# Kernel optimization log

Measured on AMD Instinct MI355X. Metric: run time of the kernel, lower is better.

## Reference

```python
import jax, jax.numpy as jnp
import numpy as np

DIM = 1024
HEADS = 16
DIM_HEAD = 64


def setup_inputs() -> dict:
    key = jax.random.key(0)
    ks = jax.random.split(key, 6)
    b, n = 2, 2048
    x = jax.random.normal(ks[0], (b, n, DIM), dtype=jnp.float32)
    gamma = jnp.ones((DIM,), dtype=jnp.float32)
    w_qkv = jax.random.normal(ks[1], (DIM, 3 * HEADS * DIM_HEAD), dtype=jnp.float32) * (DIM ** -0.5)
    w_gates = jax.random.normal(ks[2], (DIM, HEADS), dtype=jnp.float32) * (DIM ** -0.5)
    b_gates = jnp.zeros((HEADS,), dtype=jnp.float32)
    w_out = jax.random.normal(ks[3], (HEADS * DIM_HEAD, DIM), dtype=jnp.float32) * ((HEADS * DIM_HEAD) ** -0.5)
    freqs = jax.random.uniform(ks[4], (DIM_HEAD // 2,), dtype=jnp.float32)
    return {"x": x, "gamma": gamma, "w_qkv": w_qkv, "w_gates": w_gates,
            "b_gates": b_gates, "w_out": w_out, "freqs": freqs}


def _rotate_half(t):
    # interleaved pairs: (x1, x2) -> (-x2, x1)
    tp = t.reshape(t.shape[:-1] + (t.shape[-1] // 2, 2))
    x1, x2 = tp[..., 0], tp[..., 1]
    return jnp.stack((-x2, x1), axis=-1).reshape(t.shape)


def reference(x, gamma, w_qkv, w_gates, b_gates, w_out, freqs):
    b, n, d = x.shape
    # RMSNorm variant: divide by L2 norm, scale by gamma * sqrt(dim)
    xn = x / jnp.linalg.norm(x, axis=-1, keepdims=True)
    xn = xn * gamma * (d ** 0.5)
    # QKV projection: (b, n, 3*H*D) -> q,k,v each (b, h, n, dh)
    qkv = xn @ w_qkv
    qkv = qkv.reshape(b, n, 3, HEADS, DIM_HEAD).transpose(2, 0, 3, 1, 4)
    q, k, v = qkv[0], qkv[1], qkv[2]
    # Inline RoPE (interleaved): freqs (n, dh)
    pos = jnp.arange(n, dtype=freqs.dtype)
    f = jnp.repeat(pos[:, None] * freqs[None, :], 2, axis=-1)  # (n, dh)
    cos_f, sin_f = jnp.cos(f), jnp.sin(f)
    q = q * cos_f + _rotate_half(q) * sin_f
    k = k * cos_f + _rotate_half(k) * sin_f
    # SDPA
    scale = DIM_HEAD ** -0.5
    scores = jnp.einsum('bhqd,bhkd->bhqk', q, k) * scale
    attn = jax.nn.softmax(scores, axis=-1)
    out = jnp.einsum('bhqk,bhkd->bhqd', attn, v)  # (b, h, n, dh)
    # per-head sigmoid gate from normalized input
    gates = xn @ w_gates + b_gates  # (b, n, h)
    out = out * jax.nn.sigmoid(gates.transpose(0, 2, 1))[..., None]
    # merge heads and output projection
    out = out.transpose(0, 2, 1, 3).reshape(b, n, HEADS * DIM_HEAD)
    return out @ w_out
```

## Files before the change

### kernel.cpp

```cpp
#include <hip/hip_runtime.h>

typedef __bf16 bf16_t;
typedef __bf16 bf16x8 __attribute__((ext_vector_type(8)));
typedef __bf16 bf16x4 __attribute__((ext_vector_type(4)));
typedef float f32x4 __attribute__((ext_vector_type(4)));

#define B_  2
#define N_  2048
#define D_  1024
#define H_  16
#define DH_ 64

#define GLL16(g, l) __builtin_amdgcn_global_load_lds( \
    (const __attribute__((address_space(1))) void*)(g), \
    (__attribute__((address_space(3))) void*)(l), 16, 0, 0)

__global__ __launch_bounds__(256) void k_rmsnorm(const float* __restrict__ x,
    const float* __restrict__ gamma, bf16_t* __restrict__ xn) {
  int row = blockIdx.x;
  const float4* xr = (const float4*)(x + (size_t)row * D_);
  int tid = threadIdx.x;
  float4 v = xr[tid];
  float ss = v.x*v.x + v.y*v.y + v.z*v.z + v.w*v.w;
  #pragma unroll
  for (int off = 32; off > 0; off >>= 1) ss += __shfl_down(ss, off);
  __shared__ float red[4];
  if ((tid & 63) == 0) red[tid >> 6] = ss;
  __syncthreads();
  float scale = 32.0f * rsqrtf(red[0] + red[1] + red[2] + red[3]);
  float4 g = ((const float4*)gamma)[tid];
  bf16x4 o;
  o[0] = (bf16_t)(v.x * scale * g.x);
  o[1] = (bf16_t)(v.y * scale * g.y);
  o[2] = (bf16_t)(v.z * scale * g.z);
  o[3] = (bf16_t)(v.w * scale * g.w);
  *(bf16x4*)(xn + (size_t)row * D_ + tid * 4) = o;
}

__global__ __launch_bounds__(256) void k_transpose_cvt(const float* __restrict__ W,
    bf16_t* __restrict__ Wt, int R, int C) {
  __shared__ float tile[32][33];
  int c0 = blockIdx.x * 32, r0 = blockIdx.y * 32;
  int tx = threadIdx.x & 31, ty = threadIdx.x >> 5;
  #pragma unroll
  for (int i = 0; i < 4; ++i) {
    int r = ty + i * 8;
    tile[r][tx] = W[(size_t)(r0 + r) * C + c0 + tx];
  }
  __syncthreads();
  #pragma unroll
  for (int i = 0; i < 4; ++i) {
    int rr = ty + i * 8;
    Wt[(size_t)(c0 + rr) * R + r0 + tx] = (bf16_t)tile[tx][rr];
  }
}

template<bool OUT_BF16>
__global__ __launch_bounds__(256) void k_gemm_bt(const bf16_t* __restrict__ A,
    const bf16_t* __restrict__ Bt, void* __restrict__ Cp, int M, int N, int K) {
  constexpr int BK = 32;
  __shared__ __align__(16) bf16_t As[128 * BK];
  __shared__ __align__(16) bf16_t Bs[128 * BK];
  int tid = threadIdx.x, wave = tid >> 6, lane = tid & 63;
  int l16 = lane & 15, quad = lane >> 4;
  int bm = blockIdx.x * 128, bn = blockIdx.y * 128;
  int wm = (wave >> 1) * 64, wn = (wave & 1) * 64;
  int srow = wave * 32 + (lane >> 2);
  int scol = (lane & 3) * 8;
  const bf16_t* gA0 = &A [(size_t)(bm + srow)      * K + scol];
  const bf16_t* gA1 = &A [(size_t)(bm + srow + 16) * K + scol];
  const bf16_t* gB0 = &Bt[(size_t)(bn + srow)      * K + scol];
  const bf16_t* gB1 = &Bt[(size_t)(bn + srow + 16) * K + scol];
  bf16_t* lA0 = &As[(wave * 32)      * BK];
  bf16_t* lA1 = &As[(wave * 32 + 16) * BK];
  bf16_t* lB0 = &Bs[(wave * 32)      * BK];
  bf16_t* lB1 = &Bs[(wave * 32 + 16) * BK];
  f32x4 acc[4][4] = {};
  for (int k0 = 0; k0 < K; k0 += BK) {
    GLL16(gA0 + k0, lA0);
    GLL16(gA1 + k0, lA1);
    GLL16(gB0 + k0, lB0);
    GLL16(gB1 + k0, lB1);
    __syncthreads();
    bf16x8 af[4], bfr[4];
    #pragma unroll
    for (int t = 0; t < 4; ++t) {
      af[t]  = *(const bf16x8*)&As[(wm + t * 16 + l16) * BK + quad * 8];
      bfr[t] = *(const bf16x8*)&Bs[(wn + t * 16 + l16) * BK + quad * 8];
    }
    #pragma unroll
    for (int mt = 0; mt < 4; ++mt)
      #pragma unroll
      for (int nt = 0; nt < 4; ++nt)
        acc[mt][nt] = __builtin_amdgcn_mfma_f32_16x16x32_bf16(af[mt], bfr[nt], acc[mt][nt], 0, 0, 0);
    __syncthreads();
  }
  #pragma unroll
  for (int mt = 0; mt < 4; ++mt)
    #pragma unroll
    for (int nt = 0; nt < 4; ++nt)
      #pragma unroll
      for (int r = 0; r < 4; ++r) {
        int row = bm + wm + mt * 16 + quad * 4 + r;
        int col = bn + wn + nt * 16 + l16;
        float v = acc[mt][nt][r];
        if (OUT_BF16) ((bf16_t*)Cp)[(size_t)row * N + col] = (bf16_t)v;
        else          ((float*)Cp)[(size_t)row * N + col] = v;
      }
}

__global__ __launch_bounds__(256) void k_rope(const bf16_t* __restrict__ qkvb,
    const float* __restrict__ freqs, bf16_t* __restrict__ Qb, bf16_t* __restrict__ Kb) {
  int row = blockIdx.x, b = row >> 11, n = row & 2047;
  __shared__ float cs[32], sn[32];
  int tid = threadIdx.x;
  if (tid < 32) { float f = (float)n * freqs[tid]; cs[tid] = cosf(f); sn[tid] = sinf(f); }
  __syncthreads();
  const bf16_t* src = qkvb + (size_t)row * 3072;
  #pragma unroll
  for (int it = 0; it < 2; ++it) {
    int p = tid + 256 * it;
    int h = p >> 5, j = p & 31;
    size_t dst = ((size_t)(b * H_ + h) * N_ + n) * DH_ + 2 * j;
    float c = cs[j], s = sn[j];
    {
      float v0 = (float)src[h * 64 + 2 * j], v1 = (float)src[h * 64 + 2 * j + 1];
      union { bf16_t q[2]; unsigned u; } pk;
      pk.q[0] = (bf16_t)((v0 * c - v1 * s) * 0.125f);
      pk.q[1] = (bf16_t)((v1 * c + v0 * s) * 0.125f);
      *(unsigned*)&Qb[dst] = pk.u;
    }
    {
      float v0 = (float)src[1024 + h * 64 + 2 * j], v1 = (float)src[1024 + h * 64 + 2 * j + 1];
      union { bf16_t q[2]; unsigned u; } pk;
      pk.q[0] = (bf16_t)(v0 * c - v1 * s);
      pk.q[1] = (bf16_t)(v1 * c + v0 * s);
      *(unsigned*)&Kb[dst] = pk.u;
    }
  }
}

__global__ __launch_bounds__(256) void k_vtrans(const bf16_t* __restrict__ qkvb,
    bf16_t* __restrict__ Vb) {
  __shared__ bf16_t Vs[64][72];
  int bh = blockIdx.x, nt = blockIdx.y;
  int b = bh >> 4, h = bh & 15;
  int n0 = nt * 64;
  int tid = threadIdx.x;
  #pragma unroll
  for (int it = 0; it < 2; ++it) {
    int chunk = tid + 256 * it;
    int nl = chunk >> 3, c = (chunk & 7) * 8;
    *(bf16x8*)&Vs[nl][c] =
        *(const bf16x8*)&qkvb[(size_t)(b * N_ + n0 + nl) * 3072 + 2048 + h * 64 + c];
  }
  __syncthreads();
  #pragma unroll
  for (int it = 0; it < 2; ++it) {
    int chunk = tid + 256 * it;
    int d = chunk >> 3, nc = (chunk & 7) * 8;
    bf16x8 o;
    #pragma unroll
    for (int jj = 0; jj < 8; ++jj) o[jj] = Vs[nc + jj][d];
    *(bf16x8*)&Vb[((size_t)bh * DH_ + d) * N_ + n0 + nc] = o;
  }
}

__global__ __launch_bounds__(256) void k_gates(const bf16_t* __restrict__ xn,
    const float* __restrict__ wg, const float* __restrict__ bg,
    float* __restrict__ gsig) {
  int row = blockIdx.x;
  int tid = threadIdx.x;
  int h = tid & 15, seg = tid >> 4;
  const bf16_t* xr = xn + (size_t)row * D_;
  float part = 0.f;
  #pragma unroll 8
  for (int j = 0; j < 64; ++j) {
    int i = seg * 64 + j;
    part += (float)xr[i] * wg[i * 16 + h];
  }
  __shared__ float red[16][17];
  red[seg][h] = part;
  __syncthreads();
  if (tid < 16) {
    float s = bg[tid];
    #pragma unroll
    for (int sg = 0; sg < 16; ++sg) s += red[sg][tid];
    gsig[(size_t)row * 16 + tid] = 1.0f / (1.0f + __expf(-s));
  }
}

__global__ __launch_bounds__(256) void k_flash(const bf16_t* __restrict__ Qb,
    const bf16_t* __restrict__ Kb, const bf16_t* __restrict__ Vb,
    const float* __restrict__ gsig, bf16_t* __restrict__ Ao) {
  __shared__ __align__(16) bf16_t Ks[64 * 72];
  __shared__ __align__(16) bf16_t Vt[64 * 72];
  __shared__ __align__(16) bf16_t Ps[4][32 * 72];
  int bh = blockIdx.y, b = bh >> 4, h = bh & 15;
  int tid = threadIdx.x, wave = tid >> 6, lane = tid & 63;
  int l16 = lane & 15, quad = lane >> 4;
  int qw = blockIdx.x * 128 + wave * 32;
  const bf16_t* Qh = Qb + (size_t)bh * N_ * DH_;
  const bf16_t* Kh = Kb + (size_t)bh * N_ * DH_;
  const bf16_t* Vh = Vb + (size_t)bh * DH_ * N_;
  bf16_t* Pw = Ps[wave];
  bf16x8 qf[2][2];
  #pragma unroll
  for (int qt = 0; qt < 2; ++qt)
    #pragma unroll
    for (int hf = 0; hf < 2; ++hf)
      qf[qt][hf] = *(const bf16x8*)&Qh[(size_t)(qw + qt * 16 + l16) * DH_ + hf * 32 + quad * 8];
  f32x4 accO[2][4] = {};
  float lsum[2] = {0.f, 0.f};
  int sk = tid >> 3;
  int sc = (tid & 7) * 8;
  for (int k0 = 0; k0 < N_; k0 += 64) {
    *(bf16x8*)&Ks[sk * 72 + sc]        = *(const bf16x8*)&Kh[(size_t)(k0 + sk) * DH_ + sc];
    *(bf16x8*)&Ks[(sk + 32) * 72 + sc] = *(const bf16x8*)&Kh[(size_t)(k0 + sk + 32) * DH_ + sc];
    *(bf16x8*)&Vt[sk * 72 + sc]        = *(const bf16x8*)&Vh[(size_t)sk * N_ + k0 + sc];
    *(bf16x8*)&Vt[(sk + 32) * 72 + sc] = *(const bf16x8*)&Vh[(size_t)(sk + 32) * N_ + k0 + sc];
    __syncthreads();
    f32x4 st[4][2];
    #pragma unroll
    for (int kt = 0; kt < 4; ++kt) {
      bf16x8 kf0 = *(const bf16x8*)&Ks[(kt * 16 + l16) * 72 + quad * 8];
      bf16x8 kf1 = *(const bf16x8*)&Ks[(kt * 16 + l16) * 72 + 32 + quad * 8];
      #pragma unroll
      for (int qt = 0; qt < 2; ++qt) {
        f32x4 z = {};
        z = __builtin_amdgcn_mfma_f32_16x16x32_bf16(kf0, qf[qt][0], z, 0, 0, 0);
        z = __builtin_amdgcn_mfma_f32_16x16x32_bf16(kf1, qf[qt][1], z, 0, 0, 0);
        st[kt][qt] = z;
      }
    }
    #pragma unroll
    for (int qt = 0; qt < 2; ++qt)
      #pragma unroll
      for (int kt = 0; kt < 4; ++kt) {
        bf16x4 pk;
        #pragma unroll
        for (int r = 0; r < 4; ++r) {
          float p = __expf(st[kt][qt][r] - 8.0f);
          lsum[qt] += p;
          pk[r] = (bf16_t)p;
        }
        *(bf16x4*)&Pw[(qt * 16 + l16) * 72 + kt * 16 + quad * 4] = pk;
      }
    bf16x8 pf[2][2];
    #pragma unroll
    for (int qt = 0; qt < 2; ++qt)
      #pragma unroll
      for (int hf = 0; hf < 2; ++hf)
        pf[qt][hf] = *(const bf16x8*)&Pw[(qt * 16 + l16) * 72 + hf * 32 + quad * 8];
    #pragma unroll
    for (int dt = 0; dt < 4; ++dt)
      #pragma unroll
      for (int hf = 0; hf < 2; ++hf) {
        bf16x8 vf = *(const bf16x8*)&Vt[(dt * 16 + l16) * 72 + hf * 32 + quad * 8];
        #pragma unroll
        for (int qt = 0; qt < 2; ++qt)
          accO[qt][dt] = __builtin_amdgcn_mfma_f32_16x16x32_bf16(pf[qt][hf], vf, accO[qt][dt], 0, 0, 0);
      }
    __syncthreads();
  }
  float lfull[2];
  #pragma unroll
  for (int qt = 0; qt < 2; ++qt) {
    float s = lsum[qt];
    s += __shfl_xor(s, 16);
    s += __shfl_xor(s, 32);
    lfull[qt] = s;
  }
  #pragma unroll
  for (int qt = 0; qt < 2; ++qt)
    #pragma unroll
    for (int r = 0; r < 4; ++r) {
      int qs = quad * 4 + r;
      float l_e = __shfl(lfull[qt], qs);
      int q = qw + qt * 16 + qs;
      float g = gsig[((size_t)b * N_ + q) * H_ + h];
      float ginv = g / l_e;
      #pragma unroll
      for (int dt = 0; dt < 4; ++dt)
        Ao[((size_t)b * N_ + q) * (H_ * DH_) + h * DH_ + dt * 16 + l16] =
            (bf16_t)(accO[qt][dt][r] * ginv);
    }
}

extern "C" void kernel_launch(void* const* d_in, const int* in_sizes, int n_in,
                              void* d_out, int out_size, void* d_ws, size_t ws_size,
                              hipStream_t stream) {
  (void)in_sizes; (void)n_in; (void)out_size; (void)ws_size;
  const float* x      = (const float*)d_in[0];
  const float* gamma  = (const float*)d_in[1];
  const float* w_qkv  = (const float*)d_in[2];
  const float* w_gate = (const float*)d_in[3];
  const float* b_gate = (const float*)d_in[4];
  const float* w_out  = (const float*)d_in[5];
  const float* freqs  = (const float*)d_in[6];
  float* out = (float*)d_out;
  char* ws = (char*)d_ws;
  bf16_t* xn    = (bf16_t*)(ws);
  bf16_t* wqkvT = (bf16_t*)(ws + ((size_t)8  << 20));
  bf16_t* woutT = (bf16_t*)(ws + ((size_t)14 << 20));
  bf16_t* Qb    = (bf16_t*)(ws + ((size_t)16 << 20));
  bf16_t* Kb    = (bf16_t*)(ws + ((size_t)24 << 20));
  bf16_t* Vb    = (bf16_t*)(ws + ((size_t)32 << 20));
  float*  gsig  = (float*) (ws + ((size_t)40 << 20));
  bf16_t* attn  = (bf16_t*)(ws + ((size_t)41 << 20));
  bf16_t* qkvb  = (bf16_t*)(ws + ((size_t)49 << 20));

  k_transpose_cvt<<<dim3(3072 / 32, 1024 / 32), 256, 0, stream>>>(w_qkv, wqkvT, 1024, 3072);
  k_transpose_cvt<<<dim3(1024 / 32, 1024 / 32), 256, 0, stream>>>(w_out, woutT, 1024, 1024);
  k_rmsnorm<<<4096, 256, 0, stream>>>(x, gamma, xn);
  k_gemm_bt<true><<<dim3(32, 24), 256, 0, stream>>>(xn, wqkvT, (void*)qkvb, 4096, 3072, 1024);
  k_rope<<<4096, 256, 0, stream>>>(qkvb, freqs, Qb, Kb);
  k_vtrans<<<dim3(32, 32), 256, 0, stream>>>(qkvb, Vb);
  k_gates<<<4096, 256, 0, stream>>>(xn, w_gate, b_gate, gsig);
  k_flash<<<dim3(16, 32), 256, 0, stream>>>(Qb, Kb, Vb, gsig, attn);
  k_gemm_bt<false><<<dim3(32, 8), 256, 0, stream>>>(attn, woutT, (void*)out, 4096, 1024, 1024);
}
```

Measured before the change: 253.0 us.

## Fuse RoPE and V transpose into QKV GEMM, split flash over keys, retile output GEMM

The QKV GEMM epilogue now applies RoPE to Q and K, using a precomputed cos/sin table, and writes V directly in transposed layout. This removes the bf16 qkv intermediate and the separate rope and vtrans kernels. Flash attention is split into two key halves per query block, which doubles the grid. It writes fp32 partial outputs and row sums, and a new merge kernel combines them and applies the sigmoid gate. The output projection uses 64-row tiles to launch more blocks. The merge adds fp32 partial traffic and is correct only if both halves share the same softmax max reference.

```diff
diff --git a/kernel.cpp b/kernel.cpp
--- a/kernel.cpp
+++ b/kernel.cpp
@@ -14,6 +14,14 @@
 #define GLL16(g, l) __builtin_amdgcn_global_load_lds( \
     (const __attribute__((address_space(1))) void*)(g), \
     (__attribute__((address_space(3))) void*)(l), 16, 0, 0)
+
+__global__ __launch_bounds__(256) void k_trig(const float* __restrict__ freqs,
+    float2* __restrict__ trig) {
+  int i = blockIdx.x * 256 + threadIdx.x;
+  int n = i >> 5, j = i & 31;
+  float f = (float)n * freqs[j];
+  trig[i] = make_float2(cosf(f), sinf(f));
+}
 
 __global__ __launch_bounds__(256) void k_rmsnorm(const float* __restrict__ x,
     const float* __restrict__ gamma, bf16_t* __restrict__ xn) {
@@ -55,10 +63,10 @@
   }
 }
 
-template<bool OUT_BF16>
-__global__ __launch_bounds__(256) void k_gemm_bt(const bf16_t* __restrict__ A,
-    const bf16_t* __restrict__ Bt, void* __restrict__ Cp, int M, int N, int K) {
-  constexpr int BK = 32;
+__global__ __launch_bounds__(256) void k_gemm_qkv(const bf16_t* __restrict__ A,
+    const bf16_t* __restrict__ Bt, const float2* __restrict__ trig,
+    bf16_t* __restrict__ Qb, bf16_t* __restrict__ Kb, bf16_t* __restrict__ Vb) {
+  constexpr int BK = 32, K = 1024;
   __shared__ __align__(16) bf16_t As[128 * BK];
   __shared__ __align__(16) bf16_t Bs[128 * BK];
   int tid = threadIdx.x, wave = tid >> 6, lane = tid & 63;
@@ -95,75 +103,94 @@
         acc[mt][nt] = __builtin_amdgcn_mfma_f32_16x16x32_bf16(af[mt], bfr[nt], acc[mt][nt], 0, 0, 0);
     __syncthreads();
   }
-  #pragma unroll
-  for (int mt = 0; mt < 4; ++mt)
+  int type = bn >> 10;
+  int h = (((bn & 1023) + wn) >> 6);
+  if (type < 2) {
+    bf16_t* dst = (type == 0) ? Qb : Kb;
+    float qsc = (type == 0) ? 0.125f : 1.0f;
+    #pragma unroll
+    for (int nt = 0; nt < 4; ++nt) {
+      int d = nt * 16 + l16;
+      int j = d >> 1;
+      bool odd = (d & 1);
+      #pragma unroll
+      for (int mt = 0; mt < 4; ++mt)
+        #pragma unroll
+        for (int r = 0; r < 4; ++r) {
+          int row = bm + wm + mt * 16 + quad * 4 + r;
+          int b = row >> 11, n = row & 2047;
+          float v = acc[mt][nt][r];
+          float vp = __shfl_xor(v, 1);
+          float2 cs = trig[n * 32 + j];
+          float o = odd ? (v * cs.x + vp * cs.y) : (v * cs.x - vp * cs.y);
+          dst[((size_t)(b * H_ + h) * N_ + n) * DH_ + d] = (bf16_t)(o * qsc);
+        }
+    }
+  } else {
+    #pragma unroll
+    for (int mt = 0; mt < 4; ++mt) {
+      int row0 = bm + wm + mt * 16 + quad * 4;
+      int b = row0 >> 11, n0 = row0 & 2047;
+      #pragma unroll
+      for (int nt = 0; nt < 4; ++nt) {
+        int d = nt * 16 + l16;
+        bf16x4 pk;
+        #pragma unroll
+        for (int r = 0; r < 4; ++r) pk[r] = (bf16_t)acc[mt][nt][r];
+        *(bf16x4*)&Vb[((size_t)(b * H_ + h) * DH_ + d) * N_ + n0] = pk;
+      }
+    }
+  }
+}
+
+__global__ __launch_bounds__(256) void k_gemm_out(const bf16_t* __restrict__ A,
+    const bf16_t* __restrict__ Bt, float* __restrict__ C, int M, int N, int K) {
+  constexpr int BK = 32;
+  __shared__ __align__(16) bf16_t As[64 * BK];
+  __shared__ __align__(16) bf16_t Bs[128 * BK];
+  int tid = threadIdx.x, wave = tid >> 6, lane = tid & 63;
+  int l16 = lane & 15, quad = lane >> 4;
+  int bm = blockIdx.x * 64, bn = blockIdx.y * 128;
+  int wm = (wave >> 1) * 32, wn = (wave & 1) * 64;
+  int srowA = wave * 16 + (lane >> 2);
+  int srowB = wave * 32 + (lane >> 2);
+  int scol = (lane & 3) * 8;
+  const bf16_t* gA0 = &A [(size_t)(bm + srowA)      * K + scol];
+  const bf16_t* gB0 = &Bt[(size_t)(bn + srowB)      * K + scol];
+  const bf16_t* gB1 = &Bt[(size_t)(bn + srowB + 16) * K + scol];
+  bf16_t* lA0 = &As[(wave * 16)      * BK];
+  bf16_t* lB0 = &Bs[(wave * 32)      * BK];
+  bf16_t* lB1 = &Bs[(wave * 32 + 16) * BK];
+  f32x4 acc[2][4] = {};
+  for (int k0 = 0; k0 < K; k0 += BK) {
+    GLL16(gA0 + k0, lA0);
+    GLL16(gB0 + k0, lB0);
+    GLL16(gB1 + k0, lB1);
+    __syncthreads();
+    bf16x8 af[2], bfr[4];
+    #pragma unroll
+    for (int t = 0; t < 2; ++t)
+      af[t] = *(const bf16x8*)&As[(wm + t * 16 + l16) * BK + quad * 8];
+    #pragma unroll
+    for (int t = 0; t < 4; ++t)
+      bfr[t] = *(const bf16x8*)&Bs[(wn + t * 16 + l16) * BK + quad * 8];
+    #pragma unroll
+    for (int mt = 0; mt < 2; ++mt)
+      #pragma unroll
+      for (int nt = 0; nt < 4; ++nt)
+        acc[mt][nt] = __builtin_amdgcn_mfma_f32_16x16x32_bf16(af[mt], bfr[nt], acc[mt][nt], 0, 0, 0);
+    __syncthreads();
+  }
+  #pragma unroll
+  for (int mt = 0; mt < 2; ++mt)
     #pragma unroll
     for (int nt = 0; nt < 4; ++nt)
       #pragma unroll
       for (int r = 0; r < 4; ++r) {
         int row = bm + wm + mt * 16 + quad * 4 + r;
         int col = bn + wn + nt * 16 + l16;
-        float v = acc[mt][nt][r];
-        if (OUT_BF16) ((bf16_t*)Cp)[(size_t)row * N + col] = (bf16_t)v;
-        else          ((float*)Cp)[(size_t)row * N + col] = v;
-      }
-}
-
-__global__ __launch_bounds__(256) void k_rope(const bf16_t* __restrict__ qkvb,
-    const float* __restrict__ freqs, bf16_t* __restrict__ Qb, bf16_t* __restrict__ Kb) {
-  int row = blockIdx.x, b = row >> 11, n = row & 2047;
-  __shared__ float cs[32], sn[32];
-  int tid = threadIdx.x;
-  if (tid < 32) { float f = (float)n * freqs[tid]; cs[tid] = cosf(f); sn[tid] = sinf(f); }
-  __syncthreads();
-  const bf16_t* src = qkvb + (size_t)row * 3072;
-  #pragma unroll
-  for (int it = 0; it < 2; ++it) {
-    int p = tid + 256 * it;
-    int h = p >> 5, j = p & 31;
-    size_t dst = ((size_t)(b * H_ + h) * N_ + n) * DH_ + 2 * j;
-    float c = cs[j], s = sn[j];
-    {
-      float v0 = (float)src[h * 64 + 2 * j], v1 = (float)src[h * 64 + 2 * j + 1];
-      union { bf16_t q[2]; unsigned u; } pk;
-      pk.q[0] = (bf16_t)((v0 * c - v1 * s) * 0.125f);
-      pk.q[1] = (bf16_t)((v1 * c + v0 * s) * 0.125f);
-      *(unsigned*)&Qb[dst] = pk.u;
-    }
-    {
-      float v0 = (float)src[1024 + h * 64 + 2 * j], v1 = (float)src[1024 + h * 64 + 2 * j + 1];
-      union { bf16_t q[2]; unsigned u; } pk;
-      pk.q[0] = (bf16_t)(v0 * c - v1 * s);
-      pk.q[1] = (bf16_t)(v1 * c + v0 * s);
-      *(unsigned*)&Kb[dst] = pk.u;
-    }
-  }
-}
-
-__global__ __launch_bounds__(256) void k_vtrans(const bf16_t* __restrict__ qkvb,
-    bf16_t* __restrict__ Vb) {
-  __shared__ bf16_t Vs[64][72];
-  int bh = blockIdx.x, nt = blockIdx.y;
-  int b = bh >> 4, h = bh & 15;
-  int n0 = nt * 64;
-  int tid = threadIdx.x;
-  #pragma unroll
-  for (int it = 0; it < 2; ++it) {
-    int chunk = tid + 256 * it;
-    int nl = chunk >> 3, c = (chunk & 7) * 8;
-    *(bf16x8*)&Vs[nl][c] =
-        *(const bf16x8*)&qkvb[(size_t)(b * N_ + n0 + nl) * 3072 + 2048 + h * 64 + c];
-  }
-  __syncthreads();
-  #pragma unroll
-  for (int it = 0; it < 2; ++it) {
-    int chunk = tid + 256 * it;
-    int d = chunk >> 3, nc = (chunk & 7) * 8;
-    bf16x8 o;
-    #pragma unroll
-    for (int jj = 0; jj < 8; ++jj) o[jj] = Vs[nc + jj][d];
-    *(bf16x8*)&Vb[((size_t)bh * DH_ + d) * N_ + n0 + nc] = o;
-  }
+        C[(size_t)row * N + col] = acc[mt][nt][r];
+      }
 }
 
 __global__ __launch_bounds__(256) void k_gates(const bf16_t* __restrict__ xn,
@@ -192,11 +219,12 @@
 
 __global__ __launch_bounds__(256) void k_flash(const bf16_t* __restrict__ Qb,
     const bf16_t* __restrict__ Kb, const bf16_t* __restrict__ Vb,
-    const float* __restrict__ gsig, bf16_t* __restrict__ Ao) {
+    float* __restrict__ Op0, float* __restrict__ Op1, float* __restrict__ Lpart) {
   __shared__ __align__(16) bf16_t Ks[64 * 72];
   __shared__ __align__(16) bf16_t Vt[64 * 72];
   __shared__ __align__(16) bf16_t Ps[4][32 * 72];
   int bh = blockIdx.y, b = bh >> 4, h = bh & 15;
+  int split = blockIdx.z;
   int tid = threadIdx.x, wave = tid >> 6, lane = tid & 63;
   int l16 = lane & 15, quad = lane >> 4;
   int qw = blockIdx.x * 128 + wave * 32;
@@ -214,7 +242,8 @@
   float lsum[2] = {0.f, 0.f};
   int sk = tid >> 3;
   int sc = (tid & 7) * 8;
-  for (int k0 = 0; k0 < N_; k0 += 64) {
+  int kbeg = split * (N_ / 2), kend = kbeg + N_ / 2;
+  for (int k0 = kbeg; k0 < kend; k0 += 64) {
     *(bf16x8*)&Ks[sk * 72 + sc]        = *(const bf16x8*)&Kh[(size_t)(k0 + sk) * DH_ + sc];
     *(bf16x8*)&Ks[(sk + 32) * 72 + sc] = *(const bf16x8*)&Kh[(size_t)(k0 + sk + 32) * DH_ + sc];
     *(bf16x8*)&Vt[sk * 72 + sc]        = *(const bf16x8*)&Vh[(size_t)sk * N_ + k0 + sc];
@@ -271,20 +300,40 @@
     s += __shfl_xor(s, 32);
     lfull[qt] = s;
   }
-  #pragma unroll
-  for (int qt = 0; qt < 2; ++qt)
+  float* Op = (split == 0) ? Op0 : Op1;
+  #pragma unroll
+  for (int qt = 0; qt < 2; ++qt) {
+    if (quad == 0) {
+      int q = qw + qt * 16 + l16;
+      Lpart[(size_t)split * 65536 + ((size_t)b * N_ + q) * H_ + h] = lfull[qt];
+    }
     #pragma unroll
     for (int r = 0; r < 4; ++r) {
-      int qs = quad * 4 + r;
-      float l_e = __shfl(lfull[qt], qs);
-      int q = qw + qt * 16 + qs;
-      float g = gsig[((size_t)b * N_ + q) * H_ + h];
-      float ginv = g / l_e;
+      int q = qw + qt * 16 + quad * 4 + r;
+      size_t base = ((size_t)b * N_ + q) * 1024 + h * DH_;
       #pragma unroll
       for (int dt = 0; dt < 4; ++dt)
-        Ao[((size_t)b * N_ + q) * (H_ * DH_) + h * DH_ + dt * 16 + l16] =
-            (bf16_t)(accO[qt][dt][r] * ginv);
-    }
+        Op[base + dt * 16 + l16] = accO[qt][dt][r];
+    }
+  }
+}
+
+__global__ __launch_bounds__(256) void k_merge(const float* __restrict__ Op0,
+    const float* __restrict__ Op1, const float* __restrict__ Lpart,
+    const float* __restrict__ gsig, bf16_t* __restrict__ attn) {
+  int row = blockIdx.x, tid = threadIdx.x;
+  int col = tid * 4, h = col >> 6;
+  float l = Lpart[(size_t)row * H_ + h] + Lpart[65536 + (size_t)row * H_ + h];
+  float g = gsig[(size_t)row * H_ + h];
+  float sc = g / l;
+  float4 a0 = *(const float4*)&Op0[(size_t)row * 1024 + col];
+  float4 a1 = *(const float4*)&Op1[(size_t)row * 1024 + col];
+  bf16x4 o;
+  o[0] = (bf16_t)((a0.x + a1.x) * sc);
+  o[1] = (bf16_t)((a0.y + a1.y) * sc);
+  o[2] = (bf16_t)((a0.z + a1.z) * sc);
+  o[3] = (bf16_t)((a0.w + a1.w) * sc);
+  *(bf16x4*)&attn[(size_t)row * 1024 + col] = o;
 }
 
 extern "C" void kernel_launch(void* const* d_in, const int* in_sizes, int n_in,
@@ -302,21 +351,24 @@
   char* ws = (char*)d_ws;
   bf16_t* xn    = (bf16_t*)(ws);
   bf16_t* wqkvT = (bf16_t*)(ws + ((size_t)8  << 20));
-  bf16_t* woutT = (bf16_t*)(ws + ((size_t)14 << 20));
+  float*  Opart0= (float*) (ws);
   bf16_t* Qb    = (bf16_t*)(ws + ((size_t)16 << 20));
   bf16_t* Kb    = (bf16_t*)(ws + ((size_t)24 << 20));
   bf16_t* Vb    = (bf16_t*)(ws + ((size_t)32 << 20));
   float*  gsig  = (float*) (ws + ((size_t)40 << 20));
   bf16_t* attn  = (bf16_t*)(ws + ((size_t)41 << 20));
-  bf16_t* qkvb  = (bf16_t*)(ws + ((size_t)49 << 20));
-
+  float*  Opart1= (float*) (ws + ((size_t)49 << 20));
+  float*  Lpart = (float*) (ws + ((size_t)65 << 20));
+  bf16_t* woutT = (bf16_t*)(ws + ((size_t)66 << 20));
+  float2* trig  = (float2*)(ws + ((size_t)68 << 20));
+
+  k_trig<<<256, 256, 0, stream>>>(freqs, trig);
   k_transpose_cvt<<<dim3(3072 / 32, 1024 / 32), 256, 0, stream>>>(w_qkv, wqkvT, 1024, 3072);
   k_transpose_cvt<<<dim3(1024 / 32, 1024 / 32), 256, 0, stream>>>(w_out, woutT, 1024, 1024);
   k_rmsnorm<<<4096, 256, 0, stream>>>(x, gamma, xn);
-  k_gemm_bt<true><<<dim3(32, 24), 256, 0, stream>>>(xn, wqkvT, (void*)qkvb, 4096, 3072, 1024);
-  k_rope<<<4096, 256, 0, stream>>>(qkvb, freqs, Qb, Kb);
-  k_vtrans<<<dim3(32, 32), 256, 0, stream>>>(qkvb, Vb);
+  k_gemm_qkv<<<dim3(32, 24), 256, 0, stream>>>(xn, wqkvT, trig, Qb, Kb, Vb);
   k_gates<<<4096, 256, 0, stream>>>(xn, w_gate, b_gate, gsig);
-  k_flash<<<dim3(16, 32), 256, 0, stream>>>(Qb, Kb, Vb, gsig, attn);
-  k_gemm_bt<false><<<dim3(32, 8), 256, 0, stream>>>(attn, woutT, (void*)out, 4096, 1024, 1024);
-}
+  k_flash<<<dim3(16, 32, 2), 256, 0, stream>>>(Qb, Kb, Vb, Opart0, Opart1, Lpart);
+  k_merge<<<4096, 256, 0, stream>>>(Opart0, Opart1, Lpart, gsig, attn);
+  k_gemm_out<<<dim3(64, 8), 256, 0, stream>>>(attn, woutT, out, 4096, 1024, 1024);
+}
```

Measured after the change: 261.8 us. 3.5% more time.
